# Optimization experiments

Measured on AMD Instinct MI355X. Metric: run time of the kernel, lower is better.

## Reference

```python
import jax, jax.numpy as jnp
import numpy as np

N_NODES = 100000
N_EDGES = 1600000
IN_FEATS = 128
HIDDEN = 64
OUT_FEATS = 64
N_LABELS = 8


def setup_inputs() -> dict:
    key = jax.random.key(0)
    ks = jax.random.split(key, 10)
    glorot = lambda k, fi, fo: jax.random.normal(k, (fi, fo), jnp.float32) * jnp.sqrt(2.0 / (fi + fo))
    return {
        "features": jax.random.normal(ks[0], (N_NODES, IN_FEATS), jnp.float32),
        "edge_src": jax.random.randint(ks[1], (N_EDGES,), 0, N_NODES, jnp.int32),
        "edge_dst": jax.random.randint(ks[2], (N_EDGES,), 0, N_NODES, jnp.int32),
        "edge_types": jax.random.randint(ks[3], (N_EDGES,), 0, 4, jnp.int32),
        "W1": glorot(ks[4], IN_FEATS, HIDDEN),
        "b1": jnp.zeros((HIDDEN,), jnp.float32),
        "W2": glorot(ks[5], HIDDEN, OUT_FEATS),
        "b2": jnp.zeros((OUT_FEATS,), jnp.float32),
        "Wp": glorot(ks[6], OUT_FEATS, N_LABELS),
        "bp": jnp.zeros((N_LABELS,), jnp.float32),
    }


def _degree_norms(edge_src, edge_dst, n_nodes):
    ones = jnp.ones(edge_src.shape[0], jnp.float32)
    deg_out = jax.ops.segment_sum(ones, edge_src, num_segments=n_nodes)
    deg_in = jax.ops.segment_sum(ones, edge_dst, num_segments=n_nodes)
    # DGL clamps degrees to min 1 before pow(-0.5)
    norm_src = jnp.maximum(deg_out, 1.0) ** -0.5  # [N]
    norm_dst = jnp.maximum(deg_in, 1.0) ** -0.5   # [N]
    return norm_src, norm_dst


def _graph_conv(x, W, b, edge_src, edge_dst, norm_src, norm_dst, n_nodes):
    # norm='both': scale src, dense transform first (mult_first), aggregate, scale dst
    h = (x * norm_src[:, None]) @ W            # [N, out]
    msg = h[edge_src]                          # [E, out] gather
    agg = jax.ops.segment_sum(msg, edge_dst, num_segments=n_nodes)  # [N, out] scatter-add
    return agg * norm_dst[:, None] + b


def reference(features, edge_src, edge_dst, edge_types, W1, b1, W2, b2, Wp, bp):
    n_nodes = features.shape[0]
    norm_src, norm_dst = _degree_norms(edge_src, edge_dst, n_nodes)
    x = jax.nn.relu(_graph_conv(features, W1, b1, edge_src, edge_dst, norm_src, norm_dst, n_nodes))
    # dropout is identity in eval mode
    x = jax.nn.relu(_graph_conv(x, W2, b2, edge_src, edge_dst, norm_src, norm_dst, n_nodes))
    logits = x @ Wp + bp                       # [N, n_labels]
    return jax.nn.softmax(logits, axis=1)
```

## Files before the change

kernel.cpp:

```cpp
#include <hip/hip_runtime.h>
#include <hip/hip_fp16.h>
#include <math.h>


#define NODES   100000
#define INF     128
#define HID     64
#define NLAB    8

#define SB      512
#define NSB     ((NODES + SB - 1) / SB)
#define NHALF   ((NODES + 255) / 256)
#define SCAP    9000
#define CAPH    4600
#define PCHUNK  8192
#define B1T     1024
#define B2T     1024
#define PEPT    (PCHUNK / B1T)
#define SRCMASK 0x1FFFF
#define GSTRIDE 16

#define WCVT_ELEMS (64 * (INF + 8) + 64 * (HID + 8))
#define WCVT_WGS   ((WCVT_ELEMS + B1T - 1) / B1T)

union H8 { int4 i4; __half2 h2[4]; unsigned int u[4]; };

typedef _Float16 half8 __attribute__((ext_vector_type(8)));
typedef float floatx4 __attribute__((ext_vector_type(4)));

__device__ __forceinline__ void fma_mixs2(float& a0, float& a1, unsigned int h2, float s) {
    asm("v_fma_mix_f32 %0, %2, %3, %0 op_sel_hi:[1,0,0]\n\t"
        "v_fma_mix_f32 %1, %2, %3, %1 op_sel:[1,0,0] op_sel_hi:[1,0,0]"
        : "+v"(a0), "+v"(a1) : "v"(h2), "v"(s));
}


__global__ __launch_bounds__(B1T)
void build1_kernel(const int* __restrict__ src, const int* __restrict__ dst,
                   int* __restrict__ gcur_d, int* __restrict__ gcur_s,
                   int* __restrict__ dreg, unsigned short* __restrict__ sreg,
                   int E, int partWGs,
                   const float* __restrict__ W1, const float* __restrict__ W2,
                   _Float16* __restrict__ wt1, _Float16* __restrict__ wt2) {
    __shared__ int hd[NHALF], bd[NHALF], hs[NSB], bs[NSB];
    const int tid = threadIdx.x;

    if (blockIdx.x >= partWGs) {
        const int N1 = 64 * (INF + 8);
        const int N2 = 64 * (HID + 8);
        int i = (blockIdx.x - partWGs) * B1T + tid;
        if (i < N1) {
            int n = i / (INF + 8), k = i % (INF + 8);
            wt1[i] = (k < INF) ? (_Float16)W1[k * 64 + n] : (_Float16)0.f;
        } else if (i < N1 + N2) {
            int j = i - N1;
            int n = j / (HID + 8), k = j % (HID + 8);
            wt2[j] = (k < HID) ? (_Float16)W2[k * 64 + n] : (_Float16)0.f;
        }
        return;
    }

    const int e0 = blockIdx.x * PCHUNK;

    for (int i = tid; i < NHALF; i += B1T) { hd[i] = 0; }
    for (int i = tid; i < NSB; i += B1T) { hs[i] = 0; }
    __syncthreads();

    int es[PEPT], ed[PEPT];
#pragma unroll
    for (int i = 0; i < PEPT; ++i) {
        int e = e0 + tid + i * B1T;
        if (e < E) {
            es[i] = src[e]; ed[i] = dst[e];
            atomicAdd(&hd[ed[i] >> 8], 1);
            atomicAdd(&hs[es[i] >> 9], 1);
        } else es[i] = -1;
    }
    __syncthreads();

    if (tid < NHALF) {
        int c = hd[tid]; bd[tid] = c ? atomicAdd(&gcur_d[tid * GSTRIDE], c) : 0;
    }
    if (tid < NSB) {
        int c = hs[tid]; bs[tid] = c ? atomicAdd(&gcur_s[tid * GSTRIDE], c) : 0;
    }
    __syncthreads();
    for (int b = tid; b < NHALF; b += B1T) hd[b] = 0;
    for (int b = tid; b < NSB; b += B1T) hs[b] = 0;
    __syncthreads();

#pragma unroll
    for (int i = 0; i < PEPT; ++i) {
        if (es[i] >= 0) {
            int s = es[i], d = ed[i];
            int kb = d >> 8;
            int pos = bd[kb] + atomicAdd(&hd[kb], 1);
            if (pos < CAPH) dreg[(size_t)kb * CAPH + pos] = ((d & 255) << 17) | s;
            int ks = s >> 9;
            int ps = bs[ks] + atomicAdd(&hs[ks], 1);
            if (ps < SCAP) sreg[(size_t)ks * SCAP + ps] = (unsigned short)(s & (SB - 1));
        }
    }
}


__global__ __launch_bounds__(B2T)
void build2_kernel(const int* __restrict__ dreg, const int* __restrict__ gcur_d,
                   int* __restrict__ csr, int* __restrict__ starts,
                   int* __restrict__ ends, float* __restrict__ norm_d,
                   const float* __restrict__ Xv,
                   const _Float16* __restrict__ Wt, __half* __restrict__ Hh,
                   const unsigned short* __restrict__ sreg,
                   const int* __restrict__ gcur_s, float* __restrict__ norm_s,
                   int Nn) {
    __shared__ union SMem {
        int sh[SB];
        struct CS { int hist[256]; int cur[256]; int wsum[4]; int sorted[CAPH]; } c;
        _Float16 w[64 * (INF + 8)];
    } sm;
    const int tid = threadIdx.x;

    if (blockIdx.x < NSB) {
        const int sb = blockIdx.x;
        for (int i = tid; i < SB; i += B2T) sm.sh[i] = 0;
        __syncthreads();
        const int cnt = min(gcur_s[sb * GSTRIDE], SCAP);
        const unsigned short* base = sreg + (size_t)sb * SCAP;
        for (int i = tid; i < cnt; i += B2T) atomicAdd(&sm.sh[base[i]], 1);
        __syncthreads();
        for (int t = tid; t < SB; t += B2T) {
            int node = sb * SB + t;
            if (node <= Nn)
                norm_s[node] = rsqrtf(fmaxf((float)sm.sh[t], 1.0f));
        }
        return;
    }

    if (blockIdx.x < NSB + NHALF) {
        const int j = blockIdx.x - NSB;
        const int cnt = min(gcur_d[j * GSTRIDE], CAPH);
        const int* reg = dreg + (size_t)j * CAPH;

        if (tid < 256) sm.c.hist[tid] = 0;
        __syncthreads();

        for (int i = tid; i < cnt; i += B2T)
            atomicAdd(&sm.c.hist[(reg[i] >> 17) & 255], 1);
        __syncthreads();

        const int lane = tid & 63, wid = tid >> 6;
        int deg_n = 0, v = 0;
        if (tid < 256) {
            deg_n = sm.c.hist[tid];
            v = deg_n;
#pragma unroll
            for (int off = 1; off < 64; off <<= 1) {
                int u = __shfl_up(v, off, 64);
                if (lane >= off) v += u;
            }
            if (lane == 63) sm.c.wsum[wid] = v;
        }
        __syncthreads();
        if (tid < 256) {
            int wadd = 0;
#pragma unroll
            for (int q = 0; q < 3; ++q) wadd += (q < wid) ? sm.c.wsum[q] : 0;
            int st = v + wadd - deg_n;

            int node = j * 256 + tid;
            if (node < Nn) {
                int gs = j * CAPH + st;
                int dcl = min(deg_n, max(CAPH - st, 0));
                starts[node] = gs;
                ends[node]   = gs + dcl;
                norm_d[node] = rsqrtf(fmaxf((float)deg_n, 1.0f));
            }
            sm.c.cur[tid] = st;
        }
        __syncthreads();

        for (int i = tid; i < cnt; i += B2T) {
            int pe = reg[i];
            int pos = atomicAdd(&sm.c.cur[(pe >> 17) & 255], 1);
            if (pos < CAPH) sm.c.sorted[pos] = pe & SRCMASK;
        }
        __syncthreads();

        for (int i = tid; i < cnt; i += B2T) csr[(size_t)j * CAPH + i] = sm.c.sorted[i];
        return;
    }

    constexpr int K = INF;
    constexpr int KP = K + 8;
    const int bid = blockIdx.x - NSB - NHALF;

    constexpr int NI4 = 64 * KP * 2 / 16;
    for (int i = tid; i < NI4; i += B2T)
        ((int4*)sm.w)[i] = ((const int4*)Wt)[i];
    __syncthreads();

    const int w = tid >> 6, lane = tid & 63;
    const int m16 = lane & 15, quad = lane >> 4;
    const int rowA = bid * 256 + w * 16 + m16;
    const int rowC = (rowA < Nn) ? rowA : (Nn - 1);

    floatx4 acc0 = {0.f, 0.f, 0.f, 0.f};
    floatx4 acc1 = acc0, acc2 = acc0, acc3 = acc0;

#pragma unroll
    for (int c = 0; c < K / 32; ++c) {
        const int k0 = c * 32 + quad * 8;
        const float* xrow = Xv + (size_t)rowC * K;
        float4 xa = *(const float4*)(xrow + k0);
        float4 xb = *(const float4*)(xrow + k0 + 4);
        half8 a;
        a[0] = (_Float16)xa.x; a[1] = (_Float16)xa.y;
        a[2] = (_Float16)xa.z; a[3] = (_Float16)xa.w;
        a[4] = (_Float16)xb.x; a[5] = (_Float16)xb.y;
        a[6] = (_Float16)xb.z; a[7] = (_Float16)xb.w;
        half8 b0 = *(const half8*)&sm.w[(0 * 16 + m16) * KP + k0];
        half8 b1 = *(const half8*)&sm.w[(1 * 16 + m16) * KP + k0];
        half8 b2 = *(const half8*)&sm.w[(2 * 16 + m16) * KP + k0];
        half8 b3 = *(const half8*)&sm.w[(3 * 16 + m16) * KP + k0];
        acc0 = __builtin_amdgcn_mfma_f32_16x16x32_f16(a, b0, acc0, 0, 0, 0);
        acc1 = __builtin_amdgcn_mfma_f32_16x16x32_f16(a, b1, acc1, 0, 0, 0);
        acc2 = __builtin_amdgcn_mfma_f32_16x16x32_f16(a, b2, acc2, 0, 0, 0);
        acc3 = __builtin_amdgcn_mfma_f32_16x16x32_f16(a, b3, acc3, 0, 0, 0);
    }

    const int rbase = bid * 256 + w * 16 + quad * 4;
    floatx4 accs[4] = {acc0, acc1, acc2, acc3};
#pragma unroll
    for (int i = 0; i < 4; ++i) {
        int grow = rbase + i;
        if (grow < Nn) {
            __half* o = Hh + (size_t)grow * 64 + m16;
#pragma unroll
            for (int t = 0; t < 4; ++t)
                o[16 * t] = (__half)accs[t][i];
        } else if (grow == Nn) {
            __half* o = Hh + (size_t)grow * 64 + m16;
#pragma unroll
            for (int t = 0; t < 4; ++t)
                o[16 * t] = (__half)0.f;
        }
    }
}


__global__ void gather_gemm_kernel(const int* __restrict__ starts, const int* __restrict__ ends,
                                   const int* __restrict__ csr, const __half* __restrict__ Hh,
                                   const float* __restrict__ nd, const float* __restrict__ b,
                                   const float* __restrict__ ns, const _Float16* __restrict__ Wt,
                                   __half* __restrict__ Xout, int Nn) {
    constexpr int K = HID;
    constexpr int KP = K + 8;
    __shared__ _Float16 sWt[64 * KP];
    __shared__ _Float16 xt[64 * KP];

    const int tid = threadIdx.x;
    constexpr int NI4 = 64 * KP * 2 / 16;
    for (int i = tid; i < NI4; i += 256)
        ((int4*)sWt)[i] = ((const int4*)Wt)[i];

    const int lane = tid & 63;
    const int half32 = (lane >> 5) & 1;
    const int l32 = lane & 31;
    const int g = l32 >> 3;
    const int c = lane & 7;
    const int w = tid >> 6;
    const int m16 = lane & 15, quad = lane >> 4;

#pragma unroll 1
    for (int it = 0; it < 8; ++it) {
        const int nloc = w * 16 + it * 2 + half32;
        const int node = blockIdx.x * 64 + nloc;
        const int nodeC = (node < Nn) ? node : (Nn - 1);

        const int start = starts[nodeC];
        const int deg   = ends[nodeC] - start;
        const int dmax  = max(deg, __shfl_xor(deg, 32, 64));

        float acc[8] = {0.f, 0.f, 0.f, 0.f, 0.f, 0.f, 0.f, 0.f};

        for (int base = 0; base < dmax; base += 32) {
            int off = base + l32;
            int pe = (off < deg) ? csr[start + off] : Nn;
            int ecm = min(dmax - base, 32);
            int nkp = (ecm + 7) >> 3;

            for (int k = 0; k < nkp; ++k) {
                int j0 = g + 8 * k;
                int j1 = j0 + 4;
                int s0 = __shfl(pe, (lane & 32) + j0, 64);
                int s1 = __shfl(pe, (lane & 32) + j1, 64);
                float n0 = ns[s0], n1 = ns[s1];
                H8 v0, v1;
                v0.i4 = ((const int4*)(Hh + (size_t)s0 * 64))[c];
                v1.i4 = ((const int4*)(Hh + (size_t)s1 * 64))[c];
#pragma unroll
                for (int t = 0; t < 4; ++t) {
                    fma_mixs2(acc[2 * t], acc[2 * t + 1], v0.u[t], n0);
                    fma_mixs2(acc[2 * t], acc[2 * t + 1], v1.u[t], n1);
                }
            }
        }

#pragma unroll
        for (int m = 8; m <= 16; m <<= 1) {
#pragma unroll
            for (int k = 0; k < 8; ++k)
                acc[k] += __shfl_xor(acc[k], m, 64);
        }

        if (g == 0) {
            float nm = nd[nodeC];
            float4 bb0 = ((const float4*)b)[2 * c];
            float4 bb1 = ((const float4*)b)[2 * c + 1];
            H8 o;
            o.h2[0] = __floats2half2_rn(fmaxf(fmaf(acc[0], nm, bb0.x), 0.f),
                                        fmaxf(fmaf(acc[1], nm, bb0.y), 0.f));
            o.h2[1] = __floats2half2_rn(fmaxf(fmaf(acc[2], nm, bb0.z), 0.f),
                                        fmaxf(fmaf(acc[3], nm, bb0.w), 0.f));
            o.h2[2] = __floats2half2_rn(fmaxf(fmaf(acc[4], nm, bb1.x), 0.f),
                                        fmaxf(fmaf(acc[5], nm, bb1.y), 0.f));
            o.h2[3] = __floats2half2_rn(fmaxf(fmaf(acc[6], nm, bb1.z), 0.f),
                                        fmaxf(fmaf(acc[7], nm, bb1.w), 0.f));
            *(int4*)(xt + nloc * KP + c * 8) = o.i4;
        }
    }
    __syncthreads();

    const int rowL = w * 16 + m16;

    floatx4 acc0 = {0.f, 0.f, 0.f, 0.f};
    floatx4 acc1 = acc0, acc2 = acc0, acc3 = acc0;

#pragma unroll
    for (int cc = 0; cc < K / 32; ++cc) {
        const int k0 = cc * 32 + quad * 8;
        half8 a = *(const half8*)&xt[rowL * KP + k0];
        half8 b0 = *(const half8*)&sWt[(0 * 16 + m16) * KP + k0];
        half8 b1 = *(const half8*)&sWt[(1 * 16 + m16) * KP + k0];
        half8 b2 = *(const half8*)&sWt[(2 * 16 + m16) * KP + k0];
        half8 b3 = *(const half8*)&sWt[(3 * 16 + m16) * KP + k0];
        acc0 = __builtin_amdgcn_mfma_f32_16x16x32_f16(a, b0, acc0, 0, 0, 0);
        acc1 = __builtin_amdgcn_mfma_f32_16x16x32_f16(a, b1, acc1, 0, 0, 0);
        acc2 = __builtin_amdgcn_mfma_f32_16x16x32_f16(a, b2, acc2, 0, 0, 0);
        acc3 = __builtin_amdgcn_mfma_f32_16x16x32_f16(a, b3, acc3, 0, 0, 0);
    }

    const int rbase = blockIdx.x * 64 + w * 16 + quad * 4;
    floatx4 accs[4] = {acc0, acc1, acc2, acc3};
#pragma unroll
    for (int i = 0; i < 4; ++i) {
        int grow = rbase + i;
        if (grow < Nn) {
            __half* o = Xout + (size_t)grow * 64 + m16;
#pragma unroll
            for (int t = 0; t < 4; ++t)
                o[16 * t] = (__half)accs[t][i];
        } else if (grow == Nn) {
            __half* o = Xout + (size_t)grow * 64 + m16;
#pragma unroll
            for (int t = 0; t < 4; ++t)
                o[16 * t] = (__half)0.f;
        }
    }
}


__global__ void gather_proj_kernel(const int* __restrict__ starts, const int* __restrict__ ends,
                                   const int* __restrict__ csr, const __half* __restrict__ Hh,
                                   const float* __restrict__ nd, const float* __restrict__ b,
                                   const float* __restrict__ ns,
                                   const float* __restrict__ Wp, const float* __restrict__ bp,
                                   float* __restrict__ out, int Nn) {
    __shared__ float sW[NLAB * 65];
    __shared__ float sb_[NLAB];
    const int tid = threadIdx.x;

    for (int i = tid; i < 64 * NLAB; i += 256) {
        int k = i >> 3, l = i & 7;
        sW[l * 65 + k] = Wp[i];
    }
    if (tid < NLAB) sb_[tid] = bp[tid];
    __syncthreads();

    const int lane = tid & 63;
    const int half32 = (lane >> 5) & 1;
    const int l32 = lane & 31;
    const int g = l32 >> 3;
    const int c = lane & 7;

    int node = blockIdx.x * 8 + ((tid >> 6) << 1) + half32;
    const bool valid = node < Nn;
    const int nodeC = valid ? node : (Nn - 1);

    const int start = starts[nodeC];
    const int deg   = ends[nodeC] - start;
    const int dmax  = max(deg, __shfl_xor(deg, 32, 64));

    float acc[8] = {0.f, 0.f, 0.f, 0.f, 0.f, 0.f, 0.f, 0.f};

    for (int base = 0; base < dmax; base += 32) {
        int off = base + l32;
        int pe = (off < deg) ? csr[start + off] : Nn;
        int ecm = min(dmax - base, 32);
        int nkp = (ecm + 7) >> 3;

        for (int k = 0; k < nkp; ++k) {
            int j0 = g + 8 * k;
            int j1 = j0 + 4;
            int s0 = __shfl(pe, (lane & 32) + j0, 64);
            int s1 = __shfl(pe, (lane & 32) + j1, 64);
            float n0 = ns[s0], n1 = ns[s1];
            H8 v0, v1;
            v0.i4 = ((const int4*)(Hh + (size_t)s0 * 64))[c];
            v1.i4 = ((const int4*)(Hh + (size_t)s1 * 64))[c];
#pragma unroll
            for (int t = 0; t < 4; ++t) {
                fma_mixs2(acc[2 * t], acc[2 * t + 1], v0.u[t], n0);
                fma_mixs2(acc[2 * t], acc[2 * t + 1], v1.u[t], n1);
            }
        }
    }

#pragma unroll
    for (int m = 8; m <= 16; m <<= 1) {
#pragma unroll
        for (int k = 0; k < 8; ++k)
            acc[k] += __shfl_xor(acc[k], m, 64);
    }

    float nm = nd[nodeC];
    float4 b0 = ((const float4*)b)[2 * c];
    float4 b1 = ((const float4*)b)[2 * c + 1];
    float xv[8];
    xv[0] = fmaxf(fmaf(acc[0], nm, b0.x), 0.f);
    xv[1] = fmaxf(fmaf(acc[1], nm, b0.y), 0.f);
    xv[2] = fmaxf(fmaf(acc[2], nm, b0.z), 0.f);
    xv[3] = fmaxf(fmaf(acc[3], nm, b0.w), 0.f);
    xv[4] = fmaxf(fmaf(acc[4], nm, b1.x), 0.f);
    xv[5] = fmaxf(fmaf(acc[5], nm, b1.y), 0.f);
    xv[6] = fmaxf(fmaf(acc[6], nm, b1.z), 0.f);
    xv[7] = fmaxf(fmaf(acc[7], nm, b1.w), 0.f);

    const int l0 = 2 * g, l1 = l0 + 1;
    float p0 = 0.f, p1 = 0.f;
#pragma unroll
    for (int j = 0; j < 8; ++j) {
        p0 = fmaf(xv[j], sW[l0 * 65 + 8 * c + j], p0);
        p1 = fmaf(xv[j], sW[l1 * 65 + 8 * c + j], p1);
    }
    p0 += __shfl_xor(p0, 1, 64); p1 += __shfl_xor(p1, 1, 64);
    p0 += __shfl_xor(p0, 2, 64); p1 += __shfl_xor(p1, 2, 64);
    p0 += __shfl_xor(p0, 4, 64); p1 += __shfl_xor(p1, 4, 64);
    p0 += sb_[l0];
    p1 += sb_[l1];
    float mx = fmaxf(p0, p1);
    mx = fmaxf(mx, __shfl_xor(mx, 8, 64));
    mx = fmaxf(mx, __shfl_xor(mx, 16, 64));
    float e0 = __expf(p0 - mx), e1 = __expf(p1 - mx);
    float s2 = e0 + e1;
    s2 += __shfl_xor(s2, 8, 64);
    s2 += __shfl_xor(s2, 16, 64);
    float inv = 1.0f / s2;
    if (c == 0 && valid) {
        float2 o = {e0 * inv, e1 * inv};
        *(float2*)(out + (size_t)node * NLAB + l0) = o;
    }
}


extern "C" void kernel_launch(void* const* d_in, const int* in_sizes, int n_in,
                              void* d_out, int out_size, void* d_ws, size_t ws_size,
                              hipStream_t stream) {
    const float* features = (const float*)d_in[0];
    const int*   edge_src = (const int*)d_in[1];
    const int*   edge_dst = (const int*)d_in[2];
    const float* W1 = (const float*)d_in[4];
    const float* b1 = (const float*)d_in[5];
    const float* W2 = (const float*)d_in[6];
    const float* b2 = (const float*)d_in[7];
    const float* Wp = (const float*)d_in[8];
    const float* bp = (const float*)d_in[9];
    float* out = (float*)d_out;

    const int N = NODES;
    const int E = in_sizes[1];

    char* p = (char*)d_ws;
    int*   csr    = (int*)p;            p += sizeof(int) * (size_t)NHALF * CAPH;
    int*   starts = (int*)p;            p += sizeof(int) * N;
    int*   ends   = (int*)p;            p += sizeof(int) * N;
    float* norm_s = (float*)p;          p += sizeof(float) * (N + 16);
    float* norm_d = (float*)p;          p += sizeof(float) * N;
    int*   gcur_d = (int*)p;            p += sizeof(int) * NHALF * GSTRIDE;
    int*   gcur_s = (int*)p;            p += sizeof(int) * NSB * GSTRIDE;
    p = (char*)(((size_t)p + 255) & ~(size_t)255);
    _Float16* wt1 = (_Float16*)p;       p += sizeof(_Float16) * 64 * (INF + 8);
    _Float16* wt2 = (_Float16*)p;       p += sizeof(_Float16) * 64 * (HID + 8);
    p = (char*)(((size_t)p + 255) & ~(size_t)255);
    __half* h     = (__half*)p;         p += sizeof(__half) * ((size_t)N + 64) * 64;
    p = (char*)(((size_t)p + 255) & ~(size_t)255);
    __half* x     = (__half*)p;         p += sizeof(__half) * ((size_t)N + 64) * 64;
    int*            dreg = (int*)x;
    unsigned short* sreg = (unsigned short*)((char*)x + sizeof(int) * (size_t)NHALF * CAPH);

    hipMemsetAsync(gcur_d, 0, sizeof(int) * (NHALF + NSB) * GSTRIDE, stream);

    const int partWGs = (E + PCHUNK - 1) / PCHUNK;
    build1_kernel<<<partWGs + WCVT_WGS, B1T, 0, stream>>>(edge_src, edge_dst,
                                                          gcur_d, gcur_s, dreg, sreg,
                                                          E, partWGs, W1, W2, wt1, wt2);
    build2_kernel<<<NSB + NHALF + (N + 255) / 256, B2T, 0, stream>>>(dreg, gcur_d, csr,
                                                                     starts, ends, norm_d,
                                                                     features, wt1, h,
                                                                     sreg, gcur_s, norm_s, N);

    gather_gemm_kernel<<<(N + 63) / 64, 256, 0, stream>>>(starts, ends, csr, h, norm_d,
                                                          b1, norm_s, wt2, x, N);

    gather_proj_kernel<<<(N + 7) / 8, 256, 0, stream>>>(starts, ends, csr, x, norm_d,
                                                        b2, norm_s, Wp, bp, out, N);
}
```

Before: 218.6 us.

## Move layer-1 dense GEMM into edge-partition kernel, converting W1 in-block

Moves the features@W1 MFMA GEMM out of build2 and into build1 as extra workgroups that run next to the edge partitioning. Each GEMM block converts W1 to transposed fp16 straight into shared memory, so the separate wt1 buffer and its conversion pass go away. W2 conversion now runs in a single extra block. The aim is to overlap the compute-bound GEMM with the atomic-heavy partition phase and to shorten build2. In exchange, each GEMM block repeats the W1 conversion, and build1's shared memory grows to hold the union.

```diff
diff --git a/kernel.cpp b/kernel.cpp
--- a/kernel.cpp
+++ b/kernel.cpp
@@ -19,9 +19,7 @@
 #define PEPT    (PCHUNK / B1T)
 #define SRCMASK 0x1FFFF
 #define GSTRIDE 16
-
-#define WCVT_ELEMS (64 * (INF + 8) + 64 * (HID + 8))
-#define WCVT_WGS   ((WCVT_ELEMS + B1T - 1) / B1T)
+#define G1WGS   ((NODES + 255) / 256)
 
 union H8 { int4 i4; __half2 h2[4]; unsigned int u[4]; };
 
@@ -41,29 +39,87 @@
                    int* __restrict__ dreg, unsigned short* __restrict__ sreg,
                    int E, int partWGs,
                    const float* __restrict__ W1, const float* __restrict__ W2,
-                   _Float16* __restrict__ wt1, _Float16* __restrict__ wt2) {
-    __shared__ int hd[NHALF], bd[NHALF], hs[NSB], bs[NSB];
+                   _Float16* __restrict__ wt2,
+                   const float* __restrict__ Xv, __half* __restrict__ Hh, int Nn) {
+    __shared__ union SM1 {
+        struct { int hd[NHALF]; int bd[NHALF]; int hs[NSB]; int bs[NSB]; } p;
+        _Float16 w[64 * (INF + 8)];
+    } sm;
     const int tid = threadIdx.x;
 
+    if (blockIdx.x >= partWGs + G1WGS) {
+        const int N2 = 64 * (HID + 8);
+        for (int i = tid; i < N2; i += B1T) {
+            int n = i / (HID + 8), k = i % (HID + 8);
+            wt2[i] = (k < HID) ? (_Float16)W2[k * 64 + n] : (_Float16)0.f;
+        }
+        return;
+    }
+
     if (blockIdx.x >= partWGs) {
-        const int N1 = 64 * (INF + 8);
-        const int N2 = 64 * (HID + 8);
-        int i = (blockIdx.x - partWGs) * B1T + tid;
-        if (i < N1) {
-            int n = i / (INF + 8), k = i % (INF + 8);
-            wt1[i] = (k < INF) ? (_Float16)W1[k * 64 + n] : (_Float16)0.f;
-        } else if (i < N1 + N2) {
-            int j = i - N1;
-            int n = j / (HID + 8), k = j % (HID + 8);
-            wt2[j] = (k < HID) ? (_Float16)W2[k * 64 + n] : (_Float16)0.f;
+        constexpr int K = INF;
+        constexpr int KP = K + 8;
+        const int bid = blockIdx.x - partWGs;
+
+        for (int i = tid; i < 64 * KP; i += B1T) {
+            int n = i / KP, k = i % KP;
+            sm.w[i] = (k < K) ? (_Float16)W1[k * 64 + n] : (_Float16)0.f;
+        }
+        __syncthreads();
+
+        const int w = tid >> 6, lane = tid & 63;
+        const int m16 = lane & 15, quad = lane >> 4;
+        const int rowA = bid * 256 + w * 16 + m16;
+        const int rowC = (rowA < Nn) ? rowA : (Nn - 1);
+
+        floatx4 acc0 = {0.f, 0.f, 0.f, 0.f};
+        floatx4 acc1 = acc0, acc2 = acc0, acc3 = acc0;
+
+#pragma unroll
+        for (int c = 0; c < K / 32; ++c) {
+            const int k0 = c * 32 + quad * 8;
+            const float* xrow = Xv + (size_t)rowC * K;
+            float4 xa = *(const float4*)(xrow + k0);
+            float4 xb = *(const float4*)(xrow + k0 + 4);
+            half8 a;
+            a[0] = (_Float16)xa.x; a[1] = (_Float16)xa.y;
+            a[2] = (_Float16)xa.z; a[3] = (_Float16)xa.w;
+            a[4] = (_Float16)xb.x; a[5] = (_Float16)xb.y;
+            a[6] = (_Float16)xb.z; a[7] = (_Float16)xb.w;
+            half8 b0 = *(const half8*)&sm.w[(0 * 16 + m16) * KP + k0];
+            half8 b1 = *(const half8*)&sm.w[(1 * 16 + m16) * KP + k0];
+            half8 b2 = *(const half8*)&sm.w[(2 * 16 + m16) * KP + k0];
+            half8 b3 = *(const half8*)&sm.w[(3 * 16 + m16) * KP + k0];
+            acc0 = __builtin_amdgcn_mfma_f32_16x16x32_f16(a, b0, acc0, 0, 0, 0);
+            acc1 = __builtin_amdgcn_mfma_f32_16x16x32_f16(a, b1, acc1, 0, 0, 0);
+            acc2 = __builtin_amdgcn_mfma_f32_16x16x32_f16(a, b2, acc2, 0, 0, 0);
+            acc3 = __builtin_amdgcn_mfma_f32_16x16x32_f16(a, b3, acc3, 0, 0, 0);
+        }
+
+        const int rbase = bid * 256 + w * 16 + quad * 4;
+        floatx4 accs[4] = {acc0, acc1, acc2, acc3};
+#pragma unroll
+        for (int i = 0; i < 4; ++i) {
+            int grow = rbase + i;
+            if (grow < Nn) {
+                __half* o = Hh + (size_t)grow * 64 + m16;
+#pragma unroll
+                for (int t = 0; t < 4; ++t)
+                    o[16 * t] = (__half)accs[t][i];
+            } else if (grow == Nn) {
+                __half* o = Hh + (size_t)grow * 64 + m16;
+#pragma unroll
+                for (int t = 0; t < 4; ++t)
+                    o[16 * t] = (__half)0.f;
+            }
         }
         return;
     }
 
     const int e0 = blockIdx.x * PCHUNK;
 
-    for (int i = tid; i < NHALF; i += B1T) { hd[i] = 0; }
-    for (int i = tid; i < NSB; i += B1T) { hs[i] = 0; }
+    for (int i = tid; i < NHALF; i += B1T) { sm.p.hd[i] = 0; }
+    for (int i = tid; i < NSB; i += B1T) { sm.p.hs[i] = 0; }
     __syncthreads();
 
     int es[PEPT], ed[PEPT];
@@ -72,21 +128,21 @@
         int e = e0 + tid + i * B1T;
         if (e < E) {
             es[i] = src[e]; ed[i] = dst[e];
-            atomicAdd(&hd[ed[i] >> 8], 1);
-            atomicAdd(&hs[es[i] >> 9], 1);
+            atomicAdd(&sm.p.hd[ed[i] >> 8], 1);
+            atomicAdd(&sm.p.hs[es[i] >> 9], 1);
         } else es[i] = -1;
     }
     __syncthreads();
 
     if (tid < NHALF) {
-        int c = hd[tid]; bd[tid] = c ? atomicAdd(&gcur_d[tid * GSTRIDE], c) : 0;
+        int c = sm.p.hd[tid]; sm.p.bd[tid] = c ? atomicAdd(&gcur_d[tid * GSTRIDE], c) : 0;
     }
     if (tid < NSB) {
-        int c = hs[tid]; bs[tid] = c ? atomicAdd(&gcur_s[tid * GSTRIDE], c) : 0;
-    }
-    __syncthreads();
-    for (int b = tid; b < NHALF; b += B1T) hd[b] = 0;
-    for (int b = tid; b < NSB; b += B1T) hs[b] = 0;
+        int c = sm.p.hs[tid]; sm.p.bs[tid] = c ? atomicAdd(&gcur_s[tid * GSTRIDE], c) : 0;
+    }
+    __syncthreads();
+    for (int b = tid; b < NHALF; b += B1T) sm.p.hd[b] = 0;
+    for (int b = tid; b < NSB; b += B1T) sm.p.hs[b] = 0;
     __syncthreads();
 
 #pragma unroll
@@ -94,10 +150,10 @@
         if (es[i] >= 0) {
             int s = es[i], d = ed[i];
             int kb = d >> 8;
-            int pos = bd[kb] + atomicAdd(&hd[kb], 1);
+            int pos = sm.p.bd[kb] + atomicAdd(&sm.p.hd[kb], 1);
             if (pos < CAPH) dreg[(size_t)kb * CAPH + pos] = ((d & 255) << 17) | s;
             int ks = s >> 9;
-            int ps = bs[ks] + atomicAdd(&hs[ks], 1);
+            int ps = sm.p.bs[ks] + atomicAdd(&sm.p.hs[ks], 1);
             if (ps < SCAP) sreg[(size_t)ks * SCAP + ps] = (unsigned short)(s & (SB - 1));
         }
     }
@@ -108,15 +164,12 @@
 void build2_kernel(const int* __restrict__ dreg, const int* __restrict__ gcur_d,
                    int* __restrict__ csr, int* __restrict__ starts,
                    int* __restrict__ ends, float* __restrict__ norm_d,
-                   const float* __restrict__ Xv,
-                   const _Float16* __restrict__ Wt, __half* __restrict__ Hh,
                    const unsigned short* __restrict__ sreg,
                    const int* __restrict__ gcur_s, float* __restrict__ norm_s,
                    int Nn) {
     __shared__ union SMem {
         int sh[SB];
         struct CS { int hist[256]; int cur[256]; int wsum[4]; int sorted[CAPH]; } c;
-        _Float16 w[64 * (INF + 8)];
     } sm;
     const int tid = threadIdx.x;
 
@@ -136,115 +189,56 @@
         return;
     }
 
-    if (blockIdx.x < NSB + NHALF) {
-        const int j = blockIdx.x - NSB;
-        const int cnt = min(gcur_d[j * GSTRIDE], CAPH);
-        const int* reg = dreg + (size_t)j * CAPH;
-
-        if (tid < 256) sm.c.hist[tid] = 0;
-        __syncthreads();
-
-        for (int i = tid; i < cnt; i += B2T)
-            atomicAdd(&sm.c.hist[(reg[i] >> 17) & 255], 1);
-        __syncthreads();
-
-        const int lane = tid & 63, wid = tid >> 6;
-        int deg_n = 0, v = 0;
-        if (tid < 256) {
-            deg_n = sm.c.hist[tid];
-            v = deg_n;
-#pragma unroll
-            for (int off = 1; off < 64; off <<= 1) {
-                int u = __shfl_up(v, off, 64);
-                if (lane >= off) v += u;
-            }
-            if (lane == 63) sm.c.wsum[wid] = v;
-        }
-        __syncthreads();
-        if (tid < 256) {
-            int wadd = 0;
-#pragma unroll
-            for (int q = 0; q < 3; ++q) wadd += (q < wid) ? sm.c.wsum[q] : 0;
-            int st = v + wadd - deg_n;
-
-            int node = j * 256 + tid;
-            if (node < Nn) {
-                int gs = j * CAPH + st;
-                int dcl = min(deg_n, max(CAPH - st, 0));
-                starts[node] = gs;
-                ends[node]   = gs + dcl;
-                norm_d[node] = rsqrtf(fmaxf((float)deg_n, 1.0f));
-            }
-            sm.c.cur[tid] = st;
-        }
-        __syncthreads();
-
-        for (int i = tid; i < cnt; i += B2T) {
-            int pe = reg[i];
-            int pos = atomicAdd(&sm.c.cur[(pe >> 17) & 255], 1);
-            if (pos < CAPH) sm.c.sorted[pos] = pe & SRCMASK;
-        }
-        __syncthreads();
-
-        for (int i = tid; i < cnt; i += B2T) csr[(size_t)j * CAPH + i] = sm.c.sorted[i];
-        return;
-    }
-
-    constexpr int K = INF;
-    constexpr int KP = K + 8;
-    const int bid = blockIdx.x - NSB - NHALF;
-
-    constexpr int NI4 = 64 * KP * 2 / 16;
-    for (int i = tid; i < NI4; i += B2T)
-        ((int4*)sm.w)[i] = ((const int4*)Wt)[i];
-    __syncthreads();
-
-    const int w = tid >> 6, lane = tid & 63;
-    const int m16 = lane & 15, quad = lane >> 4;
-    const int rowA = bid * 256 + w * 16 + m16;
-    const int rowC = (rowA < Nn) ? rowA : (Nn - 1);
-
-    floatx4 acc0 = {0.f, 0.f, 0.f, 0.f};
-    floatx4 acc1 = acc0, acc2 = acc0, acc3 = acc0;
-
-#pragma unroll
-    for (int c = 0; c < K / 32; ++c) {
-        const int k0 = c * 32 + quad * 8;
-        const float* xrow = Xv + (size_t)rowC * K;
-        float4 xa = *(const float4*)(xrow + k0);
-        float4 xb = *(const float4*)(xrow + k0 + 4);
-        half8 a;
-        a[0] = (_Float16)xa.x; a[1] = (_Float16)xa.y;
-        a[2] = (_Float16)xa.z; a[3] = (_Float16)xa.w;
-        a[4] = (_Float16)xb.x; a[5] = (_Float16)xb.y;
-        a[6] = (_Float16)xb.z; a[7] = (_Float16)xb.w;
-        half8 b0 = *(const half8*)&sm.w[(0 * 16 + m16) * KP + k0];
-        half8 b1 = *(const half8*)&sm.w[(1 * 16 + m16) * KP + k0];
-        half8 b2 = *(const half8*)&sm.w[(2 * 16 + m16) * KP + k0];
-        half8 b3 = *(const half8*)&sm.w[(3 * 16 + m16) * KP + k0];
-        acc0 = __builtin_amdgcn_mfma_f32_16x16x32_f16(a, b0, acc0, 0, 0, 0);
-        acc1 = __builtin_amdgcn_mfma_f32_16x16x32_f16(a, b1, acc1, 0, 0, 0);
-        acc2 = __builtin_amdgcn_mfma_f32_16x16x32_f16(a, b2, acc2, 0, 0, 0);
-        acc3 = __builtin_amdgcn_mfma_f32_16x16x32_f16(a, b3, acc3, 0, 0, 0);
-    }
-
-    const int rbase = bid * 256 + w * 16 + quad * 4;
-    floatx4 accs[4] = {acc0, acc1, acc2, acc3};
-#pragma unroll
-    for (int i = 0; i < 4; ++i) {
-        int grow = rbase + i;
-        if (grow < Nn) {
-            __half* o = Hh + (size_t)grow * 64 + m16;
-#pragma unroll
-            for (int t = 0; t < 4; ++t)
-                o[16 * t] = (__half)accs[t][i];
-        } else if (grow == Nn) {
-            __half* o = Hh + (size_t)grow * 64 + m16;
-#pragma unroll
-            for (int t = 0; t < 4; ++t)
-                o[16 * t] = (__half)0.f;
-        }
-    }
+    const int j = blockIdx.x - NSB;
+    const int cnt = min(gcur_d[j * GSTRIDE], CAPH);
+    const int* reg = dreg + (size_t)j * CAPH;
+
+    if (tid < 256) sm.c.hist[tid] = 0;
+    __syncthreads();
+
+    for (int i = tid; i < cnt; i += B2T)
+        atomicAdd(&sm.c.hist[(reg[i] >> 17) & 255], 1);
+    __syncthreads();
+
+    const int lane = tid & 63, wid = tid >> 6;
+    int deg_n = 0, v = 0;
+    if (tid < 256) {
+        deg_n = sm.c.hist[tid];
+        v = deg_n;
+#pragma unroll
+        for (int off = 1; off < 64; off <<= 1) {
+            int u = __shfl_up(v, off, 64);
+            if (lane >= off) v += u;
+        }
+        if (lane == 63) sm.c.wsum[wid] = v;
+    }
+    __syncthreads();
+    if (tid < 256) {
+        int wadd = 0;
+#pragma unroll
+        for (int q = 0; q < 3; ++q) wadd += (q < wid) ? sm.c.wsum[q] : 0;
+        int st = v + wadd - deg_n;
+
+        int node = j * 256 + tid;
+        if (node < Nn) {
+            int gs = j * CAPH + st;
+            int dcl = min(deg_n, max(CAPH - st, 0));
+            starts[node] = gs;
+            ends[node]   = gs + dcl;
+            norm_d[node] = rsqrtf(fmaxf((float)deg_n, 1.0f));
+        }
+        sm.c.cur[tid] = st;
+    }
+    __syncthreads();
+
+    for (int i = tid; i < cnt; i += B2T) {
+        int pe = reg[i];
+        int pos = atomicAdd(&sm.c.cur[(pe >> 17) & 255], 1);
+        if (pos < CAPH) sm.c.sorted[pos] = pe & SRCMASK;
+    }
+    __syncthreads();
+
+    for (int i = tid; i < cnt; i += B2T) csr[(size_t)j * CAPH + i] = sm.c.sorted[i];
 }
 
 
@@ -499,7 +493,6 @@
     int*   gcur_d = (int*)p;            p += sizeof(int) * NHALF * GSTRIDE;
     int*   gcur_s = (int*)p;            p += sizeof(int) * NSB * GSTRIDE;
     p = (char*)(((size_t)p + 255) & ~(size_t)255);
-    _Float16* wt1 = (_Float16*)p;       p += sizeof(_Float16) * 64 * (INF + 8);
     _Float16* wt2 = (_Float16*)p;       p += sizeof(_Float16) * 64 * (HID + 8);
     p = (char*)(((size_t)p + 255) & ~(size_t)255);
     __half* h     = (__half*)p;         p += sizeof(__half) * ((size_t)N + 64) * 64;
@@ -511,13 +504,12 @@
     hipMemsetAsync(gcur_d, 0, sizeof(int) * (NHALF + NSB) * GSTRIDE, stream);
 
     const int partWGs = (E + PCHUNK - 1) / PCHUNK;
-    build1_kernel<<<partWGs + WCVT_WGS, B1T, 0, stream>>>(edge_src, edge_dst,
-                                                          gcur_d, gcur_s, dreg, sreg,
-                                                          E, partWGs, W1, W2, wt1, wt2);
-    build2_kernel<<<NSB + NHALF + (N + 255) / 256, B2T, 0, stream>>>(dreg, gcur_d, csr,
-                                                                     starts, ends, norm_d,
-                                                                     features, wt1, h,
-                                                                     sreg, gcur_s, norm_s, N);
+    build1_kernel<<<partWGs + G1WGS + 1, B1T, 0, stream>>>(edge_src, edge_dst,
+                                                           gcur_d, gcur_s, dreg, sreg,
+                                                           E, partWGs, W1, W2, wt2,
+                                                           features, h, N);
+    build2_kernel<<<NSB + NHALF, B2T, 0, stream>>>(dreg, gcur_d, csr, starts, ends,
+                                                   norm_d, sreg, gcur_s, norm_s, N);
 
     gather_gemm_kernel<<<(N + 63) / 64, 256, 0, stream>>>(starts, ends, csr, h, norm_d,
                                                           b1, norm_s, wt2, x, N);
```

After: 221.2 us. Within noise of the previous version (+1.2%).
